# Kernel optimization log

Measured on AMD Instinct MI355X. Metric: run time of the kernel, lower is better.

The kernel has to match this reference:

```python
import jax, jax.numpy as jnp
import numpy as np

SIGMA = 1.0
TWOPI = 2.0 * np.pi
NORM_FACTOR = 90.0474
EPS = 1e-6


def setup_inputs() -> dict:
    key = jax.random.key(0)
    k1, k2 = jax.random.split(key)
    n, n_q = 4096, 8
    q = jax.random.normal(k1, (n, n_q), dtype=jnp.float32)
    r = jax.random.normal(k2, (n, 3), dtype=jnp.float32)
    cell = jnp.zeros((1, 3, 3), dtype=jnp.float32)  # det=0 -> real-space branch
    return {"q": q, "r": r, "cell": cell}


def reference(q, r, cell):
    # Real-space Ewald term (cell is singular -> compute_potential_realspace),
    # single system (batch = None).
    n = r.shape[0]
    eye = jnp.eye(n, dtype=r.dtype)
    # pairwise displacement; epsilon on the diagonal avoids 0/0 (diagonal is masked out below)
    diff = r[None, :, :] - r[:, None, :] + EPS * eye[:, :, None]  # [n, n, 3]
    dist = jnp.linalg.norm(diff, axis=-1)                          # [n, n]
    conv = jax.scipy.special.erf(dist / (SIGMA * np.sqrt(2.0)))
    K = (conv / dist) * (1.0 - eye)  # zero self-interaction (off-diagonal mask)
    # sum_{i!=j, c} q_ic q_jc K_ij  == original pot[mask].sum()
    pot = jnp.einsum('ic,ij,jc->', q, K, q) / TWOPI / 2.0
    # remove_self_interaction=True -> no q^2 self term added
    return (pot * NORM_FACTOR)[None]  # shape [1], matches stack+sum(dim=1)
```

## Files before the change

kernel.cpp:

```cpp
#include <hip/hip_runtime.h>
#include <math.h>


#define TILE   256
#define KC     64
#define CHUNKS (TILE / KC)

__global__ __launch_bounds__(256) void ewald_pairs_kernel(
    const float* __restrict__ q,
    const float* __restrict__ r,
    float* __restrict__ partials,
    int n)
{
    __shared__ float s_q[KC][8];
    __shared__ float s_r[KC][4];
    __shared__ float s_part[4];

    const int tid = threadIdx.x;
    const int rid   = blockIdx.x / CHUNKS;
    const int chunk = blockIdx.x % CHUNKS;

    int row = (int)((sqrtf(8.0f * (float)rid + 1.0f) - 1.0f) * 0.5f);
    while ((row + 1) * (row + 2) / 2 <= rid) ++row;
    while (row * (row + 1) / 2 > rid) --row;
    const int col = rid - row * (row + 1) / 2;

    const int ti = col, tj = row;
    const bool diag = (ti == tj);

    const int i  = ti * TILE + tid;
    const int j0 = tj * TILE + chunk * KC;

    if (tid < KC * 2) {
        reinterpret_cast<float4*>(&s_q[0][0])[tid] =
            reinterpret_cast<const float4*>(q + (size_t)j0 * 8)[tid];
    }
    if (tid >= 64 && tid < 64 + KC * 3) {
        const int t = tid - 64;
        s_r[t / 3][t % 3] = r[(size_t)j0 * 3 + t];
    }
    __syncthreads();

    const float4 qa = reinterpret_cast<const float4*>(q)[(size_t)i * 2];
    const float4 qb = reinterpret_cast<const float4*>(q)[(size_t)i * 2 + 1];
    const float rx = r[(size_t)i * 3 + 0];
    const float ry = r[(size_t)i * 3 + 1];
    const float rz = r[(size_t)i * 3 + 2];

    float acc = 0.0f;

#pragma unroll 4
    for (int jj = 0; jj < KC; ++jj) {
        const float4 pa = *reinterpret_cast<const float4*>(&s_q[jj][0]);
        const float4 pb = *reinterpret_cast<const float4*>(&s_q[jj][4]);
        const float4 pr = *reinterpret_cast<const float4*>(&s_r[jj][0]);

        const float dx = pr.x - rx, dy = pr.y - ry, dz = pr.z - rz;
        const float d2 = dx * dx + dy * dy + dz * dz;

        float dot = qa.x * pa.x + qa.y * pa.y + qa.z * pa.z + qa.w * pa.w
                  + qb.x * pb.x + qb.y * pb.y + qb.z * pb.z + qb.w * pb.w;

        const float invd = __builtin_amdgcn_rsqf(d2);
        const float d    = d2 * invd;
        const float x    = d * 0.70710678118654752f;
        const float t = __builtin_amdgcn_rcpf(__builtin_fmaf(0.3275911f, x, 1.0f));
        const float e = __expf(-0.5f * d2);
        const float p = t * (0.254829592f + t * (-0.284496736f +
                        t * (1.421413741f + t * (-1.453152027f + t * 1.061405429f))));
        const float erfv = __builtin_fmaf(-p, e, 1.0f);

        const float term = dot * erfv * invd;
        const bool  ok   = (!diag) | (j0 + jj > i);
        acc += ok ? term : 0.0f;
    }

    for (int off = 32; off > 0; off >>= 1)
        acc += __shfl_down(acc, off, 64);
    if ((tid & 63) == 0) s_part[tid >> 6] = acc;
    __syncthreads();
    if (tid == 0)
        partials[blockIdx.x] = s_part[0] + s_part[1] + s_part[2] + s_part[3];
}

__global__ void finalize_kernel(const float* __restrict__ partials,
                                float* __restrict__ out, int nb) {
    const int tid = threadIdx.x;
    double s = 0.0;
    for (int idx = tid; idx < nb; idx += 64) s += (double)partials[idx];
    for (int off = 32; off > 0; off >>= 1)
        s += __shfl_down(s, off, 64);
    if (tid == 0) {
        out[0] = (float)(s * (90.0474 / 6.283185307179586));
    }
}

extern "C" void kernel_launch(void* const* d_in, const int* in_sizes, int n_in,
                              void* d_out, int out_size, void* d_ws, size_t ws_size,
                              hipStream_t stream) {
    const float* q = (const float*)d_in[0];
    const float* r = (const float*)d_in[1];
    float* out      = (float*)d_out;
    float* partials = (float*)d_ws;

    const int n  = in_sizes[1] / 3;
    const int nt = n / TILE;
    const int nrects = nt * (nt + 1) / 2;
    const int nblocks = nrects * CHUNKS;

    ewald_pairs_kernel<<<nblocks, 256, 0, stream>>>(q, r, partials, n);
    finalize_kernel<<<1, 64, 0, stream>>>(partials, out, nblocks);
}
```

Before: 75.72 us.

## Drop LDS staging, halve chunk size, template diagonal mask, widen finalize

The kernel no longer stages j-particle q and r through shared memory. Each thread reads them directly from global memory through uniform addresses, which should become scalar loads, and the block barrier is removed. KC drops from 64 to 32, doubling the block count. A template specialises the diagonal-mask branch and exp is computed through exp2. The finalize kernel now uses 256 threads with a shared-memory reduction. Together these aim to cut LDS and synchronisation overhead and raise parallelism, at the cost of more partials and per-block setup.

```diff
diff --git a/kernel.cpp b/kernel.cpp
--- a/kernel.cpp
+++ b/kernel.cpp
@@ -3,20 +3,63 @@
 
 
 #define TILE   256
-#define KC     64
+#define KC     32
 #define CHUNKS (TILE / KC)
+
+#if __has_builtin(__builtin_amdgcn_exp2f)
+#define EXP2F(x) __builtin_amdgcn_exp2f(x)
+#else
+#define EXP2F(x) __expf((x) * 0.69314718055994531f)
+#endif
+
+__device__ __forceinline__ float pair_term(float d2, float dot) {
+    const float invd = __builtin_amdgcn_rsqf(d2);
+    const float x    = d2 * invd * 0.70710678118654752f;
+    const float t = __builtin_amdgcn_rcpf(__builtin_fmaf(0.3275911f, x, 1.0f));
+    const float e = EXP2F(d2 * -0.72134752044448170f);
+    const float p = t * (0.254829592f + t * (-0.284496736f +
+                    t * (1.421413741f + t * (-1.453152027f + t * 1.061405429f))));
+    const float erfv = __builtin_fmaf(-p, e, 1.0f);
+    return dot * erfv * invd;
+}
+
+template <bool DIAG>
+__device__ __forceinline__ float rect_loop(
+    const float* __restrict__ qj, const float* __restrict__ rj,
+    const float4 qa, const float4 qb,
+    float rx, float ry, float rz, int j0, int i)
+{
+    float acc = 0.0f;
+#pragma unroll 4
+    for (int jj = 0; jj < KC; ++jj) {
+        const float dx = rj[jj * 3 + 0] - rx;
+        const float dy = rj[jj * 3 + 1] - ry;
+        const float dz = rj[jj * 3 + 2] - rz;
+        const float d2 = dx * dx + dy * dy + dz * dz;
+
+        float dot = qa.x * qj[jj * 8 + 0] + qa.y * qj[jj * 8 + 1]
+                  + qa.z * qj[jj * 8 + 2] + qa.w * qj[jj * 8 + 3]
+                  + qb.x * qj[jj * 8 + 4] + qb.y * qj[jj * 8 + 5]
+                  + qb.z * qj[jj * 8 + 6] + qb.w * qj[jj * 8 + 7];
+
+        const float term = pair_term(d2, dot);
+        if (DIAG) {
+            acc += (j0 + jj > i) ? term : 0.0f;
+        } else {
+            acc += term;
+        }
+    }
+    return acc;
+}
 
 __global__ __launch_bounds__(256) void ewald_pairs_kernel(
     const float* __restrict__ q,
     const float* __restrict__ r,
-    float* __restrict__ partials,
-    int n)
+    float* __restrict__ partials)
 {
-    __shared__ float s_q[KC][8];
-    __shared__ float s_r[KC][4];
     __shared__ float s_part[4];
 
-    const int tid = threadIdx.x;
+    const int tid   = threadIdx.x;
     const int rid   = blockIdx.x / CHUNKS;
     const int chunk = blockIdx.x % CHUNKS;
 
@@ -25,21 +68,8 @@
     while (row * (row + 1) / 2 > rid) --row;
     const int col = rid - row * (row + 1) / 2;
 
-    const int ti = col, tj = row;
-    const bool diag = (ti == tj);
-
-    const int i  = ti * TILE + tid;
-    const int j0 = tj * TILE + chunk * KC;
-
-    if (tid < KC * 2) {
-        reinterpret_cast<float4*>(&s_q[0][0])[tid] =
-            reinterpret_cast<const float4*>(q + (size_t)j0 * 8)[tid];
-    }
-    if (tid >= 64 && tid < 64 + KC * 3) {
-        const int t = tid - 64;
-        s_r[t / 3][t % 3] = r[(size_t)j0 * 3 + t];
-    }
-    __syncthreads();
+    const int i  = col * TILE + tid;
+    const int j0 = row * TILE + chunk * KC;
 
     const float4 qa = reinterpret_cast<const float4*>(q)[(size_t)i * 2];
     const float4 qb = reinterpret_cast<const float4*>(q)[(size_t)i * 2 + 1];
@@ -47,33 +77,12 @@
     const float ry = r[(size_t)i * 3 + 1];
     const float rz = r[(size_t)i * 3 + 2];
 
-    float acc = 0.0f;
+    const float* __restrict__ qj = q + (size_t)j0 * 8;
+    const float* __restrict__ rj = r + (size_t)j0 * 3;
 
-#pragma unroll 4
-    for (int jj = 0; jj < KC; ++jj) {
-        const float4 pa = *reinterpret_cast<const float4*>(&s_q[jj][0]);
-        const float4 pb = *reinterpret_cast<const float4*>(&s_q[jj][4]);
-        const float4 pr = *reinterpret_cast<const float4*>(&s_r[jj][0]);
-
-        const float dx = pr.x - rx, dy = pr.y - ry, dz = pr.z - rz;
-        const float d2 = dx * dx + dy * dy + dz * dz;
-
-        float dot = qa.x * pa.x + qa.y * pa.y + qa.z * pa.z + qa.w * pa.w
-                  + qb.x * pb.x + qb.y * pb.y + qb.z * pb.z + qb.w * pb.w;
-
-        const float invd = __builtin_amdgcn_rsqf(d2);
-        const float d    = d2 * invd;
-        const float x    = d * 0.70710678118654752f;
-        const float t = __builtin_amdgcn_rcpf(__builtin_fmaf(0.3275911f, x, 1.0f));
-        const float e = __expf(-0.5f * d2);
-        const float p = t * (0.254829592f + t * (-0.284496736f +
-                        t * (1.421413741f + t * (-1.453152027f + t * 1.061405429f))));
-        const float erfv = __builtin_fmaf(-p, e, 1.0f);
-
-        const float term = dot * erfv * invd;
-        const bool  ok   = (!diag) | (j0 + jj > i);
-        acc += ok ? term : 0.0f;
-    }
+    float acc = (col != row)
+        ? rect_loop<false>(qj, rj, qa, qb, rx, ry, rz, j0, i)
+        : rect_loop<true >(qj, rj, qa, qb, rx, ry, rz, j0, i);
 
     for (int off = 32; off > 0; off >>= 1)
         acc += __shfl_down(acc, off, 64);
@@ -83,15 +92,20 @@
         partials[blockIdx.x] = s_part[0] + s_part[1] + s_part[2] + s_part[3];
 }
 
-__global__ void finalize_kernel(const float* __restrict__ partials,
-                                float* __restrict__ out, int nb) {
+__global__ __launch_bounds__(256) void finalize_kernel(
+    const float* __restrict__ partials, float* __restrict__ out, int nb)
+{
+    __shared__ double sp[4];
     const int tid = threadIdx.x;
     double s = 0.0;
-    for (int idx = tid; idx < nb; idx += 64) s += (double)partials[idx];
+    for (int idx = tid; idx < nb; idx += 256) s += (double)partials[idx];
     for (int off = 32; off > 0; off >>= 1)
         s += __shfl_down(s, off, 64);
+    if ((tid & 63) == 0) sp[tid >> 6] = s;
+    __syncthreads();
     if (tid == 0) {
-        out[0] = (float)(s * (90.0474 / 6.283185307179586));
+        const double tot = sp[0] + sp[1] + sp[2] + sp[3];
+        out[0] = (float)(tot * (90.0474 / 6.283185307179586));
     }
 }
 
@@ -105,9 +119,9 @@
 
     const int n  = in_sizes[1] / 3;
     const int nt = n / TILE;
-    const int nrects = nt * (nt + 1) / 2;
+    const int nrects  = nt * (nt + 1) / 2;
     const int nblocks = nrects * CHUNKS;
 
-    ewald_pairs_kernel<<<nblocks, 256, 0, stream>>>(q, r, partials, n);
-    finalize_kernel<<<1, 64, 0, stream>>>(partials, out, nblocks);
+    ewald_pairs_kernel<<<nblocks, 256, 0, stream>>>(q, r, partials);
+    finalize_kernel<<<1, 256, 0, stream>>>(partials, out, nblocks);
 }
```

After: 69.15 us. 1.1x faster.
